# Kernel tuning notes

Measured on AMD Instinct MI355X. Metric: run time of the kernel, lower is better.

## Reference

```python
import jax, jax.numpy as jnp
import numpy as np

DIM = 128      # size_in
SIGN = 4       # number of leading outputs negated
CONST = 0.618  # additive constant in Linear_v5
BATCH = 4096


def setup_inputs() -> dict:
    key = jax.random.key(0)
    k0, k1, k2, k3, k4 = jax.random.split(key, 5)
    s1 = 1.0 / np.sqrt(DIM)
    s2 = 1.0 / np.sqrt(2 * DIM)
    return {
        "t": 0,
        "input_": jax.random.normal(k0, (BATCH, 2 * DIM), dtype=jnp.float32),
        "W1": jax.random.uniform(k1, (2 * DIM, DIM), jnp.float32, -s1, s1),
        "b1": jax.random.uniform(k2, (2 * DIM,), jnp.float32, -s1, s1),
        "W2": jax.random.uniform(k3, (DIM, 2 * DIM), jnp.float32, -s2, s2),
        "b2": jax.random.uniform(k4, (DIM,), jnp.float32, -s2, s2),
    }


def reference(t, input_, W1, b1, W2, b2):
    x = input_[:, :DIM]   # [B, D]
    v = input_[:, DIM:]   # [B, D]
    dtype = x.dtype
    # sign vector: first SIGN outputs of g are negated (applied after sigmoid+const)
    sgn = jnp.where(jnp.arange(DIM) < SIGN, -1.0, 1.0).astype(dtype)  # [D]

    h = x @ W1.T + b1                      # [B, 2D]
    a = jax.nn.relu(h)
    s = jax.nn.sigmoid(a @ W2.T + b2)      # [B, D]
    g = sgn * (s + CONST)                  # [B, D]

    # Analytic batch Jacobian J[b,i,j] = d g_i / d x_j
    # = sgn_i * s_i(1-s_i) * sum_k W2[i,k] * 1[h_bk>0] * W1[k,j]
    mask = (h > 0).astype(dtype)           # [B, 2D]
    Jcore = jnp.einsum('ik,bk,kj->bij', W2, mask, W1)   # [B, D, D]
    J = (sgn * (s * (1.0 - s)))[:, :, None] * Jcore      # [B, D, D]

    g_inv = 1.0 / g                        # [B, D]
    conn1 = -J * g_inv[:, None, :]         # [B, i, j] * g_inv_j
    conn2 = J * g_inv[:, :, None]          # [B, i, j] * g_inv_i

    dv_vec = v[:, :, None] * v[:, None, :]               # [B, i, j] = v_i v_j
    vtemp1 = jnp.sum((v * v)[:, :, None] * conn1, axis=1)  # sum_i v_i^2 conn1[b,i,j]
    vtemp2 = jnp.einsum('bji,bji->bj', dv_vec, conn2)
    vtemp3 = jnp.einsum('bij,bji->bj', dv_vec, conn2)
    dv = vtemp1 + vtemp2 + vtemp3          # [B, D]

    return jnp.concatenate([v, dv], axis=1)  # [B, 2D]
```

## Files before the change

kernel.cpp:

```cpp
#include <hip/hip_runtime.h>
#include <math.h>

#define DIM    128
#define DIM2   256
#define NSIGN  4
#define CCONST 0.618f
#define MB     16
#define NTHR   512

typedef short bf16x8 __attribute__((ext_vector_type(8)));
typedef float f32x4  __attribute__((ext_vector_type(4)));

#define MFMA(a,b,c) __builtin_amdgcn_mfma_f32_16x16x32_bf16((a),(b),(c),0,0,0)

union BU { uint4 q; bf16x8 b; };

__device__ __forceinline__ unsigned short f2bf(float f) {
    unsigned u = __float_as_uint(f);
    u += 0x7fffu + ((u >> 16) & 1u);
    return (unsigned short)(u >> 16);
}
__device__ __forceinline__ float bf2f(unsigned short h) {
    return __uint_as_float(((unsigned)h) << 16);
}

__device__ __forceinline__ void cvt8sp(const float* p, bf16x8& h8, bf16x8& l8) {
    union { unsigned short u[8]; bf16x8 v; } H, L;
    #pragma unroll
    for (int e = 0; e < 8; ++e) {
        float f = p[e];
        unsigned short hb = f2bf(f);
        H.u[e] = hb;
        L.u[e] = f2bf(f - bf2f(hb));
    }
    h8 = H.v; l8 = L.v;
}

__device__ __forceinline__ bf16x8 cvt8hi(const float* p) {
    union { unsigned short u[8]; bf16x8 v; } H;
    #pragma unroll
    for (int e = 0; e < 8; ++e) H.u[e] = f2bf(p[e]);
    return H.v;
}

__device__ __forceinline__ bf16x8 frag16(const unsigned short* p) {
    BU u; u.q = *(const uint4*)p; return u.b;
}

__global__ void prep_pack(const float* __restrict__ W1, const float* __restrict__ W2,
                          unsigned short* __restrict__ pk) {
    int tid  = blockIdx.x * 256 + threadIdx.x;
    int m    = tid >> 12;
    int f    = tid & 4095;
    int lane = f & 63;
    int tkt  = f >> 6;
    int r0   = ((tkt & ((m == 0 || m == 2) ? 3 : 7)) * 32) + ((lane >> 4) << 3);
    int nt   = tkt / ((m == 0 || m == 2) ? 4 : 8);
    int c    = nt * 16 + (lane & 15);

    union { uint4 q; unsigned short u[8]; } H, L;
    #pragma unroll
    for (int e = 0; e < 8; ++e) {
        int r = r0 + e;
        float v;
        if      (m == 0) v = W1[c * DIM  + r];
        else if (m == 1) v = W2[c * DIM2 + r];
        else if (m == 2) v = W2[r * DIM2 + c];
        else             v = W1[r * DIM  + c];
        unsigned short hb = f2bf(v);
        H.u[e] = hb;
        L.u[e] = f2bf(v - bf2f(hb));
    }
    size_t base = (size_t)m * 65536 + (size_t)(tkt * 64 + lane) * 8;
    *(uint4*)(pk + base) = H.q;
    if (m == 0) *(uint4*)(pk + base + 32768) = L.q;
}

__global__ __launch_bounds__(NTHR, 1)
void fused_connection(const float* __restrict__ input_,
                      const float* __restrict__ b1,
                      const float* __restrict__ b2,
                      const unsigned short* __restrict__ pk,
                      float* __restrict__ out) {
    __shared__ __align__(16) float          xv [MB][260];
    __shared__ __align__(16) unsigned short aH [MB][264];
    __shared__ __align__(16) unsigned short mwH[MB][264];
    __shared__ __align__(16) unsigned short vcH[MB][136];

    const int t    = threadIdx.x;
    const int lane = t & 63;
    const int w    = t >> 6;
    const int b0   = blockIdx.x * MB;
    const int arow = lane & 15;
    const int kg   = (lane >> 4) << 3;
    const int rbase = (lane >> 4) << 2;

    {
        int prow = t >> 5, pc = (t & 31) * 8;
        const float4* src = (const float4*)(input_ + (size_t)(b0 + prow) * DIM2 + pc);
        *(float4*)&xv[prow][pc]     = src[0];
        *(float4*)&xv[prow][pc + 4] = src[1];
    }
    __syncthreads();
    {
        int vrow = t >> 5, vc4 = (t & 31) * 4;
        *(float4*)(out + (size_t)(b0 + vrow) * DIM2 + vc4) = *(const float4*)&xv[vrow][DIM + vc4];
    }

    {
        bf16x8 xH[4], xL[4], vH[4];
        #pragma unroll
        for (int kt = 0; kt < 4; ++kt) {
            int k0 = kt * 32 + kg;
            cvt8sp(&xv[arow][k0], xH[kt], xL[kt]);
            vH[kt] = cvt8hi(&xv[arow][DIM + k0]);
        }
        #pragma unroll
        for (int nt2 = 0; nt2 < 2; ++nt2) {
            int nt = w * 2 + nt2;
            f32x4 ha = {0.f, 0.f, 0.f, 0.f};
            f32x4 wa = {0.f, 0.f, 0.f, 0.f};
            #pragma unroll
            for (int kt = 0; kt < 4; ++kt) {
                const unsigned short* bp = pk + (size_t)((nt * 4 + kt) * 64 + lane) * 8;
                bf16x8 bh = frag16(bp);
                bf16x8 bl = frag16(bp + 32768);
                ha = MFMA(xH[kt], bh, ha);
                ha = MFMA(xH[kt], bl, ha);
                ha = MFMA(xL[kt], bh, ha);
                ha = MFMA(xL[kt], bl, ha);
                wa = MFMA(vH[kt], bh, wa);
            }
            int col  = nt * 16 + arow;
            float bias = b1[col];
            #pragma unroll
            for (int reg = 0; reg < 4; ++reg) {
                int row = rbase + reg;
                float hv = ha[reg] + bias;
                bool  mk = hv > 0.f;
                aH[row][col]  = f2bf(mk ? hv : 0.f);
                mwH[row][col] = f2bf(mk ? wa[reg] : 0.f);
            }
        }
    }
    __syncthreads();

    float sreg[4];
    f32x4 t2a = {0.f, 0.f, 0.f, 0.f};
    {
        const unsigned short* p1 = pk + 65536;
        f32x4 za = {0.f, 0.f, 0.f, 0.f};
        #pragma unroll
        for (int kt = 0; kt < 8; ++kt) {
            int k0 = kt * 32 + kg;
            bf16x8 af = frag16(&aH[arow][k0]);
            bf16x8 mf = frag16(&mwH[arow][k0]);
            bf16x8 bh = frag16(p1 + (size_t)((w * 8 + kt) * 64 + lane) * 8);
            za  = MFMA(af, bh, za);
            t2a = MFMA(mf, bh, t2a);
        }
        int   ci   = w * 16 + arow;
        float sg_i = (ci < NSIGN) ? -1.f : 1.f;
        float b2v  = b2[ci];
        #pragma unroll
        for (int reg = 0; reg < 4; ++reg) {
            int row = rbase + reg;
            float z = za[reg] + b2v;
            float s = 1.f / (1.f + __expf(-z));
            sreg[reg] = s;
            float vvl = xv[row][DIM + ci];
            vcH[row][ci] = f2bf(vvl * vvl * sg_i * s * (1.f - s));
        }
    }
    __syncthreads();

    {
        const unsigned short* p2 = pk + 2 * 65536;
        bf16x8 cH[4];
        #pragma unroll
        for (int kt = 0; kt < 4; ++kt)
            cH[kt] = frag16(&vcH[arow][kt * 32 + kg]);
        #pragma unroll
        for (int nt2 = 0; nt2 < 2; ++nt2) {
            int nt = w * 2 + nt2;
            f32x4 ua = {0.f, 0.f, 0.f, 0.f};
            #pragma unroll
            for (int kt = 0; kt < 4; ++kt) {
                bf16x8 bh = frag16(p2 + (size_t)((nt * 4 + kt) * 64 + lane) * 8);
                ua = MFMA(cH[kt], bh, ua);
            }
            int ck = nt * 16 + arow;
            #pragma unroll
            for (int reg = 0; reg < 4; ++reg) {
                int row = rbase + reg;
                bool mk = aH[row][ck] != 0;
                mwH[row][ck] = f2bf(mk ? ua[reg] : 0.f);
            }
        }
    }
    __syncthreads();

    {
        const unsigned short* p3 = pk + 3 * 65536;
        f32x4 t1a = {0.f, 0.f, 0.f, 0.f};
        #pragma unroll
        for (int kt = 0; kt < 8; ++kt) {
            bf16x8 mf = frag16(&mwH[arow][kt * 32 + kg]);
            bf16x8 bh = frag16(p3 + (size_t)((w * 8 + kt) * 64 + lane) * 8);
            t1a = MFMA(mf, bh, t1a);
        }
        int   cj   = w * 16 + arow;
        float sg_j = (cj < NSIGN) ? -1.f : 1.f;
        #pragma unroll
        for (int reg = 0; reg < 4; ++reg) {
            int row = rbase + reg;
            float s  = sreg[reg];
            float cv = sg_j * s * (1.f - s);
            float gi = 1.f / (sg_j * (s + CCONST));
            float vvl = xv[row][DIM + cj];
            float dv = fmaf(-gi, t1a[reg], 2.f * vvl * gi * cv * t2a[reg]);
            out[(size_t)(b0 + row) * DIM2 + DIM + cj] = dv;
        }
    }
}

extern "C" void kernel_launch(void* const* d_in, const int* in_sizes, int n_in,
                              void* d_out, int out_size, void* d_ws, size_t ws_size,
                              hipStream_t stream) {
    const float* input_ = (const float*)d_in[1];
    const float* W1 = (const float*)d_in[2];
    const float* b1 = (const float*)d_in[3];
    const float* W2 = (const float*)d_in[4];
    const float* b2 = (const float*)d_in[5];
    float* out = (float*)d_out;
    unsigned short* pk = (unsigned short*)d_ws;

    const int batch = in_sizes[1] / DIM2;

    prep_pack<<<64, 256, 0, stream>>>(W1, W2, pk);
    fused_connection<<<batch / MB, NTHR, 0, stream>>>(input_, b1, b2, pk, out);
}
```

Baseline: 18.77 us.

## Prefetch weight fragments early, pre-convert inputs to bf16 once, drop lo*lo MFMA

Weight fragments for every GEMM stage are now loaded from global memory into registers one stage ahead, before the preceding barrier or compute. This hides load latency behind the current stage's work. Input x and v are split into bf16 hi/lo once per element during the global load and stored in shared memory. Previously each wave repeated that conversion per fragment. The xL*W1L MFMA term is also dropped, which slightly lowers precision of the first GEMM in exchange for fewer MFMAs, and register pressure rises.

```diff
diff --git a/kernel.cpp b/kernel.cpp
--- a/kernel.cpp
+++ b/kernel.cpp
@@ -23,26 +23,6 @@
 __device__ __forceinline__ float bf2f(unsigned short h) {
     return __uint_as_float(((unsigned)h) << 16);
 }
-
-__device__ __forceinline__ void cvt8sp(const float* p, bf16x8& h8, bf16x8& l8) {
-    union { unsigned short u[8]; bf16x8 v; } H, L;
-    #pragma unroll
-    for (int e = 0; e < 8; ++e) {
-        float f = p[e];
-        unsigned short hb = f2bf(f);
-        H.u[e] = hb;
-        L.u[e] = f2bf(f - bf2f(hb));
-    }
-    h8 = H.v; l8 = L.v;
-}
-
-__device__ __forceinline__ bf16x8 cvt8hi(const float* p) {
-    union { unsigned short u[8]; bf16x8 v; } H;
-    #pragma unroll
-    for (int e = 0; e < 8; ++e) H.u[e] = f2bf(p[e]);
-    return H.v;
-}
-
 __device__ __forceinline__ bf16x8 frag16(const unsigned short* p) {
     BU u; u.q = *(const uint4*)p; return u.b;
 }
@@ -82,7 +62,10 @@
                       const float* __restrict__ b2,
                       const unsigned short* __restrict__ pk,
                       float* __restrict__ out) {
-    __shared__ __align__(16) float          xv [MB][260];
+    __shared__ __align__(16) float          vv [MB][132];
+    __shared__ __align__(16) unsigned short xbH[MB][136];
+    __shared__ __align__(16) unsigned short xbL[MB][136];
+    __shared__ __align__(16) unsigned short vbH[MB][136];
     __shared__ __align__(16) unsigned short aH [MB][264];
     __shared__ __align__(16) unsigned short mwH[MB][264];
     __shared__ __align__(16) unsigned short vcH[MB][136];
@@ -95,25 +78,60 @@
     const int kg   = (lane >> 4) << 3;
     const int rbase = (lane >> 4) << 2;
 
-    {
-        int prow = t >> 5, pc = (t & 31) * 8;
+    uint4 b1hq[2][4], b1lq[2][4];
+    #pragma unroll
+    for (int nt2 = 0; nt2 < 2; ++nt2)
+        #pragma unroll
+        for (int kt = 0; kt < 4; ++kt) {
+            const unsigned short* bp = pk + (size_t)((((w * 2 + nt2) * 4 + kt) * 64 + lane) * 8);
+            b1hq[nt2][kt] = *(const uint4*)bp;
+            b1lq[nt2][kt] = *(const uint4*)(bp + 32768);
+        }
+
+    {
+        int prow = t >> 5;
+        int pc   = (t & 31) * 8;
         const float4* src = (const float4*)(input_ + (size_t)(b0 + prow) * DIM2 + pc);
-        *(float4*)&xv[prow][pc]     = src[0];
-        *(float4*)&xv[prow][pc + 4] = src[1];
-    }
-    __syncthreads();
-    {
-        int vrow = t >> 5, vc4 = (t & 31) * 4;
-        *(float4*)(out + (size_t)(b0 + vrow) * DIM2 + vc4) = *(const float4*)&xv[vrow][DIM + vc4];
-    }
-
-    {
+        float4 f0 = src[0], f1 = src[1];
+        float fa[8] = {f0.x, f0.y, f0.z, f0.w, f1.x, f1.y, f1.z, f1.w};
+        if (pc < DIM) {
+            union { unsigned short u[8]; uint4 q; } H, L;
+            #pragma unroll
+            for (int e = 0; e < 8; ++e) {
+                unsigned short hb = f2bf(fa[e]);
+                H.u[e] = hb;
+                L.u[e] = f2bf(fa[e] - bf2f(hb));
+            }
+            *(uint4*)&xbH[prow][pc] = H.q;
+            *(uint4*)&xbL[prow][pc] = L.q;
+        } else {
+            int c = pc - DIM;
+            *(float4*)&vv[prow][c]     = f0;
+            *(float4*)&vv[prow][c + 4] = f1;
+            union { unsigned short u[8]; uint4 q; } H;
+            #pragma unroll
+            for (int e = 0; e < 8; ++e) H.u[e] = f2bf(fa[e]);
+            *(uint4*)&vbH[prow][c] = H.q;
+            float4* op = (float4*)(out + (size_t)(b0 + prow) * DIM2 + c);
+            op[0] = f0; op[1] = f1;
+        }
+    }
+    __syncthreads();
+
+    uint4 b2q[8];
+    {
+        const unsigned short* p1 = pk + 65536;
+        #pragma unroll
+        for (int kt = 0; kt < 8; ++kt)
+            b2q[kt] = *(const uint4*)(p1 + (size_t)((w * 8 + kt) * 64 + lane) * 8);
+
         bf16x8 xH[4], xL[4], vH[4];
         #pragma unroll
         for (int kt = 0; kt < 4; ++kt) {
             int k0 = kt * 32 + kg;
-            cvt8sp(&xv[arow][k0], xH[kt], xL[kt]);
-            vH[kt] = cvt8hi(&xv[arow][DIM + k0]);
+            xH[kt] = frag16(&xbH[arow][k0]);
+            xL[kt] = frag16(&xbL[arow][k0]);
+            vH[kt] = frag16(&vbH[arow][k0]);
         }
         #pragma unroll
         for (int nt2 = 0; nt2 < 2; ++nt2) {
@@ -122,14 +140,13 @@
             f32x4 wa = {0.f, 0.f, 0.f, 0.f};
             #pragma unroll
             for (int kt = 0; kt < 4; ++kt) {
-                const unsigned short* bp = pk + (size_t)((nt * 4 + kt) * 64 + lane) * 8;
-                bf16x8 bh = frag16(bp);
-                bf16x8 bl = frag16(bp + 32768);
-                ha = MFMA(xH[kt], bh, ha);
-                ha = MFMA(xH[kt], bl, ha);
-                ha = MFMA(xL[kt], bh, ha);
-                ha = MFMA(xL[kt], bl, ha);
-                wa = MFMA(vH[kt], bh, wa);
+                BU bh, bl;
+                bh.q = b1hq[nt2][kt];
+                bl.q = b1lq[nt2][kt];
+                ha = MFMA(xH[kt], bh.b, ha);
+                ha = MFMA(xH[kt], bl.b, ha);
+                ha = MFMA(xL[kt], bh.b, ha);
+                wa = MFMA(vH[kt], bh.b, wa);
             }
             int col  = nt * 16 + arow;
             float bias = b1[col];
@@ -147,17 +164,24 @@
 
     float sreg[4];
     f32x4 t2a = {0.f, 0.f, 0.f, 0.f};
-    {
-        const unsigned short* p1 = pk + 65536;
+    uint4 b3q[2][4];
+    {
+        const unsigned short* p2 = pk + 2 * 65536;
+        #pragma unroll
+        for (int nt2 = 0; nt2 < 2; ++nt2)
+            #pragma unroll
+            for (int kt = 0; kt < 4; ++kt)
+                b3q[nt2][kt] = *(const uint4*)(p2 + (size_t)((((w * 2 + nt2) * 4 + kt) * 64 + lane) * 8));
+
         f32x4 za = {0.f, 0.f, 0.f, 0.f};
         #pragma unroll
         for (int kt = 0; kt < 8; ++kt) {
             int k0 = kt * 32 + kg;
             bf16x8 af = frag16(&aH[arow][k0]);
             bf16x8 mf = frag16(&mwH[arow][k0]);
-            bf16x8 bh = frag16(p1 + (size_t)((w * 8 + kt) * 64 + lane) * 8);
-            za  = MFMA(af, bh, za);
-            t2a = MFMA(mf, bh, t2a);
+            BU bh; bh.q = b2q[kt];
+            za  = MFMA(af, bh.b, za);
+            t2a = MFMA(mf, bh.b, t2a);
         }
         int   ci   = w * 16 + arow;
         float sg_i = (ci < NSIGN) ? -1.f : 1.f;
@@ -168,14 +192,19 @@
             float z = za[reg] + b2v;
             float s = 1.f / (1.f + __expf(-z));
             sreg[reg] = s;
-            float vvl = xv[row][DIM + ci];
+            float vvl = vv[row][ci];
             vcH[row][ci] = f2bf(vvl * vvl * sg_i * s * (1.f - s));
         }
     }
     __syncthreads();
 
-    {
-        const unsigned short* p2 = pk + 2 * 65536;
+    uint4 b4q[8];
+    {
+        const unsigned short* p3 = pk + 3 * 65536;
+        #pragma unroll
+        for (int kt = 0; kt < 8; ++kt)
+            b4q[kt] = *(const uint4*)(p3 + (size_t)((w * 8 + kt) * 64 + lane) * 8);
+
         bf16x8 cH[4];
         #pragma unroll
         for (int kt = 0; kt < 4; ++kt)
@@ -186,8 +215,8 @@
             f32x4 ua = {0.f, 0.f, 0.f, 0.f};
             #pragma unroll
             for (int kt = 0; kt < 4; ++kt) {
-                bf16x8 bh = frag16(p2 + (size_t)((nt * 4 + kt) * 64 + lane) * 8);
-                ua = MFMA(cH[kt], bh, ua);
+                BU bh; bh.q = b3q[nt2][kt];
+                ua = MFMA(cH[kt], bh.b, ua);
             }
             int ck = nt * 16 + arow;
             #pragma unroll
@@ -201,13 +230,12 @@
     __syncthreads();
 
     {
-        const unsigned short* p3 = pk + 3 * 65536;
         f32x4 t1a = {0.f, 0.f, 0.f, 0.f};
         #pragma unroll
         for (int kt = 0; kt < 8; ++kt) {
             bf16x8 mf = frag16(&mwH[arow][kt * 32 + kg]);
-            bf16x8 bh = frag16(p3 + (size_t)((w * 8 + kt) * 64 + lane) * 8);
-            t1a = MFMA(mf, bh, t1a);
+            BU bh; bh.q = b4q[kt];
+            t1a = MFMA(mf, bh.b, t1a);
         }
         int   cj   = w * 16 + arow;
         float sg_j = (cj < NSIGN) ? -1.f : 1.f;
@@ -217,7 +245,7 @@
             float s  = sreg[reg];
             float cv = sg_j * s * (1.f - s);
             float gi = 1.f / (sg_j * (s + CCONST));
-            float vvl = xv[row][DIM + cj];
+            float vvl = vv[row][cj];
             float dv = fmaf(-gi, t1a[reg], 2.f * vvl * gi * cv * t2a[reg]);
             out[(size_t)(b0 + row) * DIM2 + DIM + cj] = dv;
         }
```

Measured after the change: 16.71 us. -11.0%, faster.
